# Kernel tuning notes

Measured on AMD Instinct MI355X. Metric: run time of the kernel, lower is better.

Reference implementation:

```python
import jax, jax.numpy as jnp
import numpy as np

DIM = 384
HEADS = 12
CUBE = (4, 7, 7)
N = CUBE[0] * CUBE[1] * CUBE[2]  # 196
HIDDEN = 4 * DIM
BW = 256  # num_windows * batch
EPS = 1e-5


def _relative_position_index():
    c, h, w = CUBE
    coords = np.stack(np.meshgrid(np.arange(c), np.arange(h), np.arange(w), indexing='ij'))  # [3,c,h,w]
    flat = coords.reshape(3, -1)  # [3, N]
    rel = flat[:, :, None] - flat[:, None, :]  # [3, N, N]
    rel = rel.transpose(1, 2, 0).copy()
    rel[:, :, 0] += c - 1
    rel[:, :, 1] += h - 1
    rel[:, :, 2] += w - 1
    rel[:, :, 1] *= 2 * w - 1
    rel[:, :, 0] *= (2 * h - 1) * (2 * w - 1)
    return rel.sum(-1).astype(np.int32)  # [N, N]


def setup_inputs() -> dict:
    key = jax.random.key(0)
    ks = jax.random.split(key, 16)
    s = 0.02
    table_rows = (2 * CUBE[0] - 1) * (2 * CUBE[1] - 1) * (2 * CUBE[2] - 1)
    return {
        'x': jax.random.normal(ks[0], (BW, N, DIM), jnp.float32),
        'norm1_w': jnp.ones((DIM,), jnp.float32),
        'norm1_b': jnp.zeros((DIM,), jnp.float32),
        'qkv_w': jax.random.normal(ks[1], (DIM, 3 * DIM), jnp.float32) * s,
        'qkv_b': jnp.zeros((3 * DIM,), jnp.float32),
        'proj_w': jax.random.normal(ks[2], (DIM, DIM), jnp.float32) * s,
        'proj_b': jnp.zeros((DIM,), jnp.float32),
        'rpb_table': jax.random.normal(ks[3], (table_rows, HEADS), jnp.float32) * s,
        'norm2_w': jnp.ones((DIM,), jnp.float32),
        'norm2_b': jnp.zeros((DIM,), jnp.float32),
        'fc1_w': jax.random.normal(ks[4], (DIM, HIDDEN), jnp.float32) * s,
        'fc1_b': jnp.zeros((HIDDEN,), jnp.float32),
        'fc2_w': jax.random.normal(ks[5], (HIDDEN, DIM), jnp.float32) * s,
        'fc2_b': jnp.zeros((DIM,), jnp.float32),
        'rpi': jnp.asarray(_relative_position_index()),
    }


def _layernorm(x, w, b):
    mu = jnp.mean(x, axis=-1, keepdims=True)
    var = jnp.mean(jnp.square(x - mu), axis=-1, keepdims=True)
    return (x - mu) * jax.lax.rsqrt(var + EPS) * w + b


def reference(x, norm1_w, norm1_b, qkv_w, qkv_b, proj_w, proj_b, rpb_table,
              norm2_w, norm2_b, fc1_w, fc1_b, fc2_w, fc2_b, rpi):
    B_, n, C = x.shape
    hd = C // HEADS
    scale = hd ** (-0.5)

    # --- attention branch ---
    h = _layernorm(x, norm1_w, norm1_b)
    qkv = (h @ qkv_w + qkv_b).reshape(B_, n, 3, HEADS, hd)
    q, k, v = qkv[:, :, 0], qkv[:, :, 1], qkv[:, :, 2]  # [B_, n, H, hd]
    attn = jnp.einsum('bqhd,bkhd->bhqk', q * scale, k)
    bias = rpb_table[rpi]                 # [n, n, H]
    attn = attn + jnp.transpose(bias, (2, 0, 1))[None]
    attn = jax.nn.softmax(attn, axis=-1)
    out = jnp.einsum('bhqk,bkhd->bqhd', attn, v).reshape(B_, n, C)
    out = out @ proj_w + proj_b
    x = x + out

    # --- MLP branch ---
    h = _layernorm(x, norm2_w, norm2_b)
    h = jax.nn.gelu(h @ fc1_w + fc1_b, approximate=False)
    h = h @ fc2_w + fc2_b
    return x + h
```

## Files before the change

### kernel.cpp

```cpp
#include <hip/hip_runtime.h>
#include <hip/hip_bf16.h>
#include <math.h>

#define NDIM 384
#define NHEADS 12
#define NTOK 196
#define NBATCH 256
#define M_TOK (NBATCH * NTOK)
#define NHID 1536
#define THREE_DIM 1152
#define HD 32
#define EPSV 1e-5f

typedef __hip_bfloat16 bf16;
typedef __attribute__((ext_vector_type(8))) short short8;
typedef __attribute__((ext_vector_type(4))) float f32x4;

__device__ __forceinline__ void gload_lds16(const void* g, void* l) {
  __builtin_amdgcn_global_load_lds((const __attribute__((address_space(1))) void*)g,
                                   (__attribute__((address_space(3))) void*)l, 16, 0, 0);
}

__global__ void k_transpose_bf16(const float* __restrict__ src, bf16* __restrict__ dst,
                                 int K, int N) {
  int idx = blockIdx.x * 256 + threadIdx.x;
  if (idx >= K * N) return;
  int k = idx / N, n = idx - k * N;
  dst[n * K + k] = __float2bfloat16(src[idx]);
}

__global__ void k_build_bias(const float* __restrict__ table, const int* __restrict__ rpi,
                             float* __restrict__ bias_mat) {
  int idx = blockIdx.x * 256 + threadIdx.x;
  if (idx >= NTOK * NTOK) return;
  int r = rpi[idx];
#pragma unroll
  for (int h = 0; h < NHEADS; ++h)
    bias_mat[h * (NTOK * NTOK) + idx] = table[r * NHEADS + h];
}

__global__ __launch_bounds__(256) void k_layernorm(const float* __restrict__ x,
                                                   const float* __restrict__ w,
                                                   const float* __restrict__ b,
                                                   bf16* __restrict__ out) {
  int token = blockIdx.x * 4 + (threadIdx.x >> 6);
  int lane = threadIdx.x & 63;
  const float* xr = x + (size_t)token * NDIM;
  float v[6];
  float s = 0.f;
#pragma unroll
  for (int i = 0; i < 6; ++i) { v[i] = xr[lane + i * 64]; s += v[i]; }
#pragma unroll
  for (int off = 32; off >= 1; off >>= 1) s += __shfl_xor(s, off);
  float mu = s * (1.f / NDIM);
  float s2 = 0.f;
#pragma unroll
  for (int i = 0; i < 6; ++i) { float d = v[i] - mu; s2 += d * d; }
#pragma unroll
  for (int off = 32; off >= 1; off >>= 1) s2 += __shfl_xor(s2, off);
  float r = rsqrtf(s2 * (1.f / NDIM) + EPSV);
  bf16* orow = out + (size_t)token * NDIM;
#pragma unroll
  for (int i = 0; i < 6; ++i) {
    int c = lane + i * 64;
    orow[c] = __float2bfloat16((v[i] - mu) * r * w[c] + b[c]);
  }
}

template <int EPI>
__global__ __launch_bounds__(256) void k_gemm_bt(const bf16* __restrict__ A,
                                                 const bf16* __restrict__ Bt,
                                                 const float* __restrict__ bias,
                                                 const float* __restrict__ resid,
                                                 void* __restrict__ Cout,
                                                 int Nn, int K) {
  __shared__ bf16 As[128 * 32];
  __shared__ bf16 Bs[128 * 32];
  const int tid = threadIdx.x;
  const int wave = tid >> 6, lane = tid & 63;
  const int lo = lane & 15, hi = lane >> 4;
  const int wm = wave >> 1, wn = wave & 1;
  const int m0 = blockIdx.y * 128, n0 = blockIdx.x * 128;

  f32x4 acc[4][4];
#pragma unroll
  for (int i = 0; i < 4; ++i) {
#pragma unroll
    for (int j = 0; j < 4; ++j) acc[i][j] = (f32x4){0.f, 0.f, 0.f, 0.f};
  }

  const int nk = K >> 5;
  for (int ks = 0; ks < nk; ++ks) {
    int k0 = ks << 5;
#pragma unroll
    for (int it = 0; it < 2; ++it) {
      int c = it * 256 + tid;
      int row = c >> 2, part = c & 3;
      gload_lds16(A + (size_t)(m0 + row) * K + k0 + part * 8, As + c * 8);
      gload_lds16(Bt + (size_t)(n0 + row) * K + k0 + part * 8, Bs + c * 8);
    }
    __syncthreads();
    short8 af[4], bfr[4];
#pragma unroll
    for (int i = 0; i < 4; ++i) {
      af[i] = *(const short8*)(As + (wm * 64 + i * 16 + lo) * 32 + hi * 8);
      bfr[i] = *(const short8*)(Bs + (wn * 64 + i * 16 + lo) * 32 + hi * 8);
    }
#pragma unroll
    for (int i = 0; i < 4; ++i) {
#pragma unroll
      for (int j = 0; j < 4; ++j)
        acc[i][j] = __builtin_amdgcn_mfma_f32_16x16x32_bf16(af[i], bfr[j], acc[i][j], 0, 0, 0);
    }
    __syncthreads();
  }

#pragma unroll
  for (int i = 0; i < 4; ++i) {
    int r = m0 + wm * 64 + i * 16 + hi * 4;
#pragma unroll
    for (int j = 0; j < 4; ++j) {
      int cb = n0 + wn * 64 + j * 16 + lo;
      float bv = bias[cb];
#pragma unroll
      for (int e = 0; e < 4; ++e) {
        size_t idx = (size_t)(r + e) * Nn + cb;
        float val = acc[i][j][e] + bv;
        if (EPI == 1) val = 0.5f * val * (1.f + erff(val * 0.70710678118f));
        if (EPI == 2) {
          ((float*)Cout)[idx] = resid[idx] + val;
        } else {
          ((bf16*)Cout)[idx] = __float2bfloat16(val);
        }
      }
    }
  }
}

__global__ __launch_bounds__(256) void k_attn(const bf16* __restrict__ qkv,
                                              const float* __restrict__ bias_mat,
                                              bf16* __restrict__ out) {
  __shared__ __align__(16) bf16 Vt[32][232];
  __shared__ __align__(16) bf16 Ps[4][16][232];
  const int tid = threadIdx.x;
  const int wave = tid >> 6, lane = tid & 63;
  const int lo = lane & 15, hi = lane >> 4;
  const int h = blockIdx.x;
  const int b = blockIdx.y;
  const float scale = 0.17677669529663687f;
  const bf16* Kbase = qkv + (size_t)b * NTOK * THREE_DIM + NDIM + h * HD;
  const bf16* Vbase = qkv + (size_t)b * NTOK * THREE_DIM + 2 * NDIM + h * HD;
  const bf16* Qbase = qkv + (size_t)b * NTOK * THREE_DIM + h * HD;

  union U8 { short8 v; bf16 x[8]; };
  for (int u = tid; u < NTOK * 4; u += 256) {
    int t = u >> 2, dseg = (u & 3) * 8;
    U8 vv;
    vv.v = *(const short8*)(Vbase + (size_t)t * THREE_DIM + dseg);
#pragma unroll
    for (int j = 0; j < 8; ++j) Vt[dseg + j][t] = vv.x[j];
  }
  for (int u = tid; u < 32 * 28; u += 256) {
    int d = u / 28, c = 196 + u % 28;
    Vt[d][c] = __float2bfloat16(0.f);
  }
  for (int i = lane; i < 16 * 16; i += 64) {
    Ps[wave][i >> 4][208 + (i & 15)] = __float2bfloat16(0.f);
  }
  __syncthreads();

  for (int qt = wave; qt < 13; qt += 4) {
    int qrow = qt * 16 + lo;
    short8 qf = {0, 0, 0, 0, 0, 0, 0, 0};
    if (qrow < NTOK) qf = *(const short8*)(Qbase + (size_t)qrow * THREE_DIM + hi * 8);

    f32x4 s[13];
#pragma unroll
    for (int kt = 0; kt < 13; ++kt) {
      int key = kt * 16 + lo;
      short8 kf = {0, 0, 0, 0, 0, 0, 0, 0};
      if (key < NTOK) kf = *(const short8*)(Kbase + (size_t)key * THREE_DIM + hi * 8);
      f32x4 z = {0.f, 0.f, 0.f, 0.f};
      s[kt] = __builtin_amdgcn_mfma_f32_16x16x32_bf16(qf, kf, z, 0, 0, 0);
    }

#pragma unroll
    for (int e = 0; e < 4; ++e) {
      int qg = qt * 16 + hi * 4 + e;
      int qc = qg < NTOK ? qg : NTOK - 1;
      const float* brow = bias_mat + ((size_t)h * NTOK + qc) * NTOK;
      float mx = -1e30f;
#pragma unroll
      for (int kt = 0; kt < 13; ++kt) {
        int key = kt * 16 + lo;
        float v = (key < NTOK) ? (s[kt][e] * scale + brow[key]) : -1e30f;
        s[kt][e] = v;
        mx = fmaxf(mx, v);
      }
#pragma unroll
      for (int off = 8; off >= 1; off >>= 1) mx = fmaxf(mx, __shfl_xor(mx, off));
      float sm = 0.f;
#pragma unroll
      for (int kt = 0; kt < 13; ++kt) {
        float pe = __expf(s[kt][e] - mx);
        s[kt][e] = pe;
        sm += pe;
      }
#pragma unroll
      for (int off = 8; off >= 1; off >>= 1) sm += __shfl_xor(sm, off);
      float inv = 1.f / sm;
#pragma unroll
      for (int kt = 0; kt < 13; ++kt) s[kt][e] *= inv;
    }

#pragma unroll
    for (int kt = 0; kt < 13; ++kt) {
#pragma unroll
      for (int e = 0; e < 4; ++e)
        Ps[wave][hi * 4 + e][kt * 16 + lo] = __float2bfloat16(s[kt][e]);
    }

    f32x4 o[2] = {{0.f, 0.f, 0.f, 0.f}, {0.f, 0.f, 0.f, 0.f}};
#pragma unroll
    for (int c = 0; c < 7; ++c) {
      short8 pa = *(const short8*)(&Ps[wave][lo][c * 32 + hi * 8]);
#pragma unroll
      for (int n = 0; n < 2; ++n) {
        short8 vf = *(const short8*)(&Vt[n * 16 + lo][c * 32 + hi * 8]);
        o[n] = __builtin_amdgcn_mfma_f32_16x16x32_bf16(pa, vf, o[n], 0, 0, 0);
      }
    }

#pragma unroll
    for (int n = 0; n < 2; ++n) {
#pragma unroll
      for (int e = 0; e < 4; ++e) {
        int qg = qt * 16 + hi * 4 + e;
        if (qg < NTOK)
          out[(size_t)(b * NTOK + qg) * NDIM + h * HD + n * 16 + lo] = __float2bfloat16(o[n][e]);
      }
    }
  }
}

extern "C" void kernel_launch(void* const* d_in, const int* in_sizes, int n_in,
                              void* d_out, int out_size, void* d_ws, size_t ws_size,
                              hipStream_t stream) {
  const float* x       = (const float*)d_in[0];
  const float* norm1_w = (const float*)d_in[1];
  const float* norm1_b = (const float*)d_in[2];
  const float* qkv_w   = (const float*)d_in[3];
  const float* qkv_b   = (const float*)d_in[4];
  const float* proj_w  = (const float*)d_in[5];
  const float* proj_b  = (const float*)d_in[6];
  const float* rpb     = (const float*)d_in[7];
  const float* norm2_w = (const float*)d_in[8];
  const float* norm2_b = (const float*)d_in[9];
  const float* fc1_w   = (const float*)d_in[10];
  const float* fc1_b   = (const float*)d_in[11];
  const float* fc2_w   = (const float*)d_in[12];
  const float* fc2_b   = (const float*)d_in[13];
  const int*   rpi     = (const int*)d_in[14];
  float* out = (float*)d_out;

  char* ws = (char*)d_ws;
  bf16* qkv_buf = (bf16*)ws;
  bf16* mlp1 = (bf16*)ws;
  bf16* hbuf = (bf16*)(ws + 154140672);
  bf16* wqkv_t = (bf16*)(ws + 154140672 + 38535168);
  bf16* wproj_t = wqkv_t + 442368;
  bf16* wfc1_t = wproj_t + 147456;
  bf16* wfc2_t = wfc1_t + 589824;
  float* bias_mat = (float*)(wfc2_t + 589824);

  k_transpose_bf16<<<(442368 + 255) / 256, 256, 0, stream>>>(qkv_w, wqkv_t, 384, 1152);
  k_transpose_bf16<<<(147456 + 255) / 256, 256, 0, stream>>>(proj_w, wproj_t, 384, 384);
  k_transpose_bf16<<<(589824 + 255) / 256, 256, 0, stream>>>(fc1_w, wfc1_t, 384, 1536);
  k_transpose_bf16<<<(589824 + 255) / 256, 256, 0, stream>>>(fc2_w, wfc2_t, 1536, 384);
  k_build_bias<<<(NTOK * NTOK + 255) / 256, 256, 0, stream>>>(rpb, rpi, bias_mat);

  k_layernorm<<<M_TOK / 4, 256, 0, stream>>>(x, norm1_w, norm1_b, hbuf);
  k_gemm_bt<0><<<dim3(9, 392), 256, 0, stream>>>(hbuf, wqkv_t, qkv_b, nullptr, qkv_buf, 1152, 384);
  k_attn<<<dim3(NHEADS, NBATCH), 256, 0, stream>>>(qkv_buf, bias_mat, hbuf);
  k_gemm_bt<2><<<dim3(3, 392), 256, 0, stream>>>(hbuf, wproj_t, proj_b, x, out, 384, 384);
  k_layernorm<<<M_TOK / 4, 256, 0, stream>>>(out, norm2_w, norm2_b, hbuf);
  k_gemm_bt<1><<<dim3(12, 392), 256, 0, stream>>>(hbuf, wfc1_t, fc1_b, nullptr, mlp1, 1536, 384);
  k_gemm_bt<2><<<dim3(3, 392), 256, 0, stream>>>(mlp1, wfc2_t, fc2_b, out, out, 384, 1536);
}
```

Baseline: 603.9 us.

## Double-buffer GEMM LDS tiles and swizzle workgroups across XCDs

```diff
diff --git a/kernel.cpp b/kernel.cpp
--- a/kernel.cpp
+++ b/kernel.cpp
@@ -73,14 +73,17 @@
                                                  const float* __restrict__ bias,
                                                  const float* __restrict__ resid,
                                                  void* __restrict__ Cout,
-                                                 int Nn, int K) {
-  __shared__ bf16 As[128 * 32];
-  __shared__ bf16 Bs[128 * 32];
+                                                 int Nn, int K, int nbx) {
+  __shared__ bf16 As[2][128 * 32];
+  __shared__ bf16 Bs[2][128 * 32];
   const int tid = threadIdx.x;
   const int wave = tid >> 6, lane = tid & 63;
   const int lo = lane & 15, hi = lane >> 4;
   const int wm = wave >> 1, wn = wave & 1;
-  const int m0 = blockIdx.y * 128, n0 = blockIdx.x * 128;
+
+  const int nwg = gridDim.x;
+  const int swz = (blockIdx.x & 7) * (nwg >> 3) + (blockIdx.x >> 3);
+  const int m0 = (swz / nbx) * 128, n0 = (swz % nbx) * 128;
 
   f32x4 acc[4][4];
 #pragma unroll
@@ -89,22 +92,30 @@
     for (int j = 0; j < 4; ++j) acc[i][j] = (f32x4){0.f, 0.f, 0.f, 0.f};
   }
 
+  const int row = tid >> 2, part = tid & 3;
+  const int row1 = (256 + tid) >> 2, part1 = tid & 3;
+
+  gload_lds16(A + (size_t)(m0 + row) * K + part * 8, As[0] + tid * 8);
+  gload_lds16(Bt + (size_t)(n0 + row) * K + part * 8, Bs[0] + tid * 8);
+  gload_lds16(A + (size_t)(m0 + row1) * K + part1 * 8, As[0] + (256 + tid) * 8);
+  gload_lds16(Bt + (size_t)(n0 + row1) * K + part1 * 8, Bs[0] + (256 + tid) * 8);
+  __syncthreads();
+
   const int nk = K >> 5;
+  int cur = 0;
   for (int ks = 0; ks < nk; ++ks) {
-    int k0 = ks << 5;
-#pragma unroll
-    for (int it = 0; it < 2; ++it) {
-      int c = it * 256 + tid;
-      int row = c >> 2, part = c & 3;
-      gload_lds16(A + (size_t)(m0 + row) * K + k0 + part * 8, As + c * 8);
-      gload_lds16(Bt + (size_t)(n0 + row) * K + k0 + part * 8, Bs + c * 8);
-    }
-    __syncthreads();
+    if (ks + 1 < nk) {
+      int k0 = (ks + 1) << 5;
+      gload_lds16(A + (size_t)(m0 + row) * K + k0 + part * 8, As[cur ^ 1] + tid * 8);
+      gload_lds16(Bt + (size_t)(n0 + row) * K + k0 + part * 8, Bs[cur ^ 1] + tid * 8);
+      gload_lds16(A + (size_t)(m0 + row1) * K + k0 + part1 * 8, As[cur ^ 1] + (256 + tid) * 8);
+      gload_lds16(Bt + (size_t)(n0 + row1) * K + k0 + part1 * 8, Bs[cur ^ 1] + (256 + tid) * 8);
+    }
     short8 af[4], bfr[4];
 #pragma unroll
     for (int i = 0; i < 4; ++i) {
-      af[i] = *(const short8*)(As + (wm * 64 + i * 16 + lo) * 32 + hi * 8);
-      bfr[i] = *(const short8*)(Bs + (wn * 64 + i * 16 + lo) * 32 + hi * 8);
+      af[i] = *(const short8*)(As[cur] + (wm * 64 + i * 16 + lo) * 32 + hi * 8);
+      bfr[i] = *(const short8*)(Bs[cur] + (wn * 64 + i * 16 + lo) * 32 + hi * 8);
     }
 #pragma unroll
     for (int i = 0; i < 4; ++i) {
@@ -113,6 +124,7 @@
         acc[i][j] = __builtin_amdgcn_mfma_f32_16x16x32_bf16(af[i], bfr[j], acc[i][j], 0, 0, 0);
     }
     __syncthreads();
+    cur ^= 1;
   }
 
 #pragma unroll
@@ -280,10 +292,10 @@
   k_build_bias<<<(NTOK * NTOK + 255) / 256, 256, 0, stream>>>(rpb, rpi, bias_mat);
 
   k_layernorm<<<M_TOK / 4, 256, 0, stream>>>(x, norm1_w, norm1_b, hbuf);
-  k_gemm_bt<0><<<dim3(9, 392), 256, 0, stream>>>(hbuf, wqkv_t, qkv_b, nullptr, qkv_buf, 1152, 384);
+  k_gemm_bt<0><<<9 * 392, 256, 0, stream>>>(hbuf, wqkv_t, qkv_b, nullptr, qkv_buf, 1152, 384, 9);
   k_attn<<<dim3(NHEADS, NBATCH), 256, 0, stream>>>(qkv_buf, bias_mat, hbuf);
-  k_gemm_bt<2><<<dim3(3, 392), 256, 0, stream>>>(hbuf, wproj_t, proj_b, x, out, 384, 384);
+  k_gemm_bt<2><<<3 * 392, 256, 0, stream>>>(hbuf, wproj_t, proj_b, x, out, 384, 384, 3);
   k_layernorm<<<M_TOK / 4, 256, 0, stream>>>(out, norm2_w, norm2_b, hbuf);
-  k_gemm_bt<1><<<dim3(12, 392), 256, 0, stream>>>(hbuf, wfc1_t, fc1_b, nullptr, mlp1, 1536, 384);
-  k_gemm_bt<2><<<dim3(3, 392), 256, 0, stream>>>(mlp1, wfc2_t, fc2_b, out, out, 384, 1536);
-}
+  k_gemm_bt<1><<<12 * 392, 256, 0, stream>>>(hbuf, wfc1_t, fc1_b, nullptr, mlp1, 1536, 384, 12);
+  k_gemm_bt<2><<<3 * 392, 256, 0, stream>>>(mlp1, wfc2_t, fc2_b, out, out, 384, 1536, 3);
+}
```

Measured after the change: 544.2 us. -9.9%, faster.
